# Kernel optimization log

Measured on AMD Instinct MI355X. Metric: run time of the kernel, lower is better.

Reference implementation:

```python
import jax, jax.numpy as jnp
import numpy as np

B, T, N = 2048, 500, 64
DT = 0.25  # integration step
V_TH = 30.0

# Izhikevich behaviour params: (a, b, c, d, v0); u0 = b * v0
LLBN_P = (0.02, 0.20, -65.0, 6.0, -70.0)   # LLBN_behaviour (tonic-spiking-like)
EBN_P  = (0.02, 0.25, -55.0, 0.05, -64.0)  # phasic bursting
IFN_P  = (0.02, 0.25, -65.0, 6.0, -64.0)   # phasic spiking
TN_P   = (0.02, 0.20, -50.0, 2.0, -70.0)   # tonic bursting
MN_P   = IFN_P                              # phasic spiking


def izh_step(v, u, I, p):
    """One Euler step of the Izhikevich neuron; returns (spike, v_new, u_new)."""
    a, b, c, d, _ = p
    v_ = v + DT * (0.04 * v * v + 5.0 * v + 140.0 - u + I)
    u_ = u + DT * a * (b * v - u)
    z = (v_ >= V_TH).astype(v.dtype)
    v_new = jnp.where(z > 0, c, v_)
    u_new = u_ + z * d
    return z, v_new, u_new


def init_state(p, batch):
    a, b, c, d, v0 = p
    return jnp.full((batch,), v0, jnp.float32), jnp.full((batch,), b * v0, jnp.float32)


def setup_inputs() -> dict:
    key = jax.random.key(0)
    k1, k2 = jax.random.split(key)
    input_mat = jax.random.uniform(k1, (B, T, N), dtype=jnp.float32)
    weights_matrix = jax.random.uniform(k2, (24,), dtype=jnp.float32)
    return {"input_mat": input_mat, "weights_matrix": weights_matrix}


def _run(input_mat, w):
    # summed retinal drive per timestep; [B, T] -> [T, B] for scan
    zp1 = (input_mat * w[0]).sum(-1).T
    zp2 = (input_mat * w[12]).sum(-1).T

    vL, uL = init_state(LLBN_P, B); zL = jnp.zeros((B,), jnp.float32)
    vE, uE = init_state(EBN_P, B)
    vI, uI = init_state(IFN_P, B)
    vT, uT = init_state(TN_P, B); zT = jnp.zeros((B,), jnp.float32)
    vM, uM = init_state(MN_P, B)
    # channel 2 uses the SAME cells (self.LLBN/EBN/... are reused in the
    # original forward, so weights w[2],w[3],w[9],w[10] apply) with its own state
    vL2, uL2 = vL, uL; zL2 = zL
    vE2, uE2 = vE, uE
    vI2, uI2 = vI, uI
    vT2, uT2 = vT, uT; zT2 = zT
    vM2, uM2 = vM, uM

    carry0 = (vL, uL, zL, vE, uE, vI, uI, vT, uT, zT, vM, uM,
              vL2, uL2, zL2, vE2, uE2, vI2, uI2, vT2, uT2, zT2, vM2, uM2)

    def step(carry, zin):
        (vL, uL, zL, vE, uE, vI, uI, vT, uT, zT, vM, uM,
         vL2, uL2, zL2, vE2, uE2, vI2, uI2, vT2, uT2, zT2, vM2, uM2) = carry
        zp, zp2 = zin
        # --- channel 1 ---  (temp feedback is always 0 in the original: local var)
        z2, vL, uL = izh_step(vL, uL, w[2] * (zp * w[1]) + w[3] * zL, LLBN_P)
        z3, vE, uE = izh_step(vE, uE, zp * w[4] + z2 * w[5], EBN_P)
        z4, vI, uI = izh_step(vI, uI, z3 * w[6], IFN_P)
        z5, vT, uT = izh_step(vT, uT, w[9] * (z3 * w[8]) + w[10] * zT, TN_P)
        z6, vM, uM = izh_step(vM, uM, z5 * w[11], MN_P)
        # --- channel 2 ---
        z22, vL2, uL2 = izh_step(vL2, uL2, w[2] * (zp2 * w[13]) + w[3] * zL2, LLBN_P)
        z32, vE2, uE2 = izh_step(vE2, uE2, zp2 * w[16] + z22 * w[17], EBN_P)
        z42, vI2, uI2 = izh_step(vI2, uI2, z32 * w[18], IFN_P)
        z52, vT2, uT2 = izh_step(vT2, uT2, w[9] * (z32 * w[20]) + w[10] * zT2, TN_P)
        z62, vM2, uM2 = izh_step(vM2, uM2, z52 * w[23], MN_P)
        new_carry = (vL, uL, z2, vE, uE, vI, uI, vT, uT, z5, vM, uM,
                     vL2, uL2, z22, vE2, uE2, vI2, uI2, vT2, uT2, z52, vM2, uM2)
        outs = (z6, vM, z62, vM2,
                jnp.stack([z2, z3, z4, z5], -1),   # o_spikes_o [B,4]
                jnp.stack([vL, vE, vI, vT], -1))   # v_o        [B,4]
        return new_carry, outs

    _, (o_spikes, v, o_spikes2, v2, o_spikes_o, v_o) = jax.lax.scan(step, carry0, (zp1, zp2))
    # scan stacks on leading T axis -> move to [B, T, ...]
    tr = lambda a: jnp.moveaxis(a, 0, 1)
    return tr(o_spikes), tr(v), tr(o_spikes2), tr(v2), tr(o_spikes_o), tr(v_o)


def reference(input_mat, weights_matrix):
    return _run(input_mat, weights_matrix)
```

## Files before the change

kernel.cpp:

```cpp
#include <hip/hip_runtime.h>

#define B_ 2048
#define T_ 500
#define BT (B_ * T_)

__device__ __forceinline__ float izh_m(float& v, float& u, float I,
                                       float b, float c, float d, bool valid) {
    float t  = 0.04f * v * v + 5.0f * v + 140.0f - u + I;
    float v_ = v + 0.25f * t;
    float u_ = u + 0.005f * (b * v - u);
    float z  = (v_ >= 30.0f) ? 1.0f : 0.0f;
    float vn = (v_ >= 30.0f) ? c : v_;
    float un = u_ + z * d;
    if (!valid) { z = 0.f; vn = v; un = u; }
    v = vn; u = un;
    return z;
}

__device__ __forceinline__ float dpp_shr1(float x) {
    return __int_as_float(__builtin_amdgcn_update_dpp(
        0, __float_as_int(x), 0x111, 0xf, 0xf, true));
}
__device__ __forceinline__ float dpp_shr2(float x) {
    return __int_as_float(__builtin_amdgcn_update_dpp(
        0, __float_as_int(x), 0x112, 0xf, 0xf, true));
}

#define BAR() do {                                                             \
    asm volatile("s_waitcnt lgkmcnt(0)" ::: "memory");                         \
    __builtin_amdgcn_s_barrier();                                              \
    __builtin_amdgcn_sched_barrier(0);                                         \
} while (0)

__global__ __launch_bounds__(128) void fused_scan4_kernel(
        const float* __restrict__ in, const float* __restrict__ w24,
        float* __restrict__ out) {
    __shared__ float S_lds[128];
    __shared__ float ring[32 * 56];

    const int tid   = threadIdx.x;
    const int wid   = tid >> 6;
    const int lane  = tid & 63;
    const int bbase = blockIdx.x << 2;

    const int c    = lane >> 4;
    const int slot = lane & 15;
    const int chl  = slot >> 3;
    const int role = slot & 7;

    const float a0   = chl ? w24[12] : w24[0];
    const float W1v  = chl ? w24[13] : w24[1];
    const float W4v  = chl ? w24[16] : w24[4];
    const float W5x  = chl ? w24[17] : w24[5];
    const float W6v  = chl ? w24[18] : w24[6];
    const float W8v  = chl ? w24[20] : w24[8];
    const float W11v = chl ? w24[23] : w24[11];
    const float W2 = w24[2], W3 = w24[3], W9 = w24[9], W10 = w24[10];

    float pb, pcc, pd, v, u, wA, wB, wC, wD;
    float fL = 0.f, fE = 0.f, fITM = 0.f;
    float sel1 = 0.f, sel2 = 0.f;
    int offs;
    if (role == 0) {
        pb=0.20f; pcc=-65.f; pd=6.f;   v=-70.f; u=-14.f;
        wA=W2;  wB=W1v;  wC=0.f; wD=W3;  offs=0; fL=1.f;
    } else if (role == 1) {
        pb=0.25f; pcc=-55.f; pd=0.05f; v=-64.f; u=-16.f;
        wA=1.f; wB=W4v;  wC=W5x; wD=0.f; offs=3; fE=1.f; sel1=1.f;
    } else if (role == 2) {
        pb=0.25f; pcc=-65.f; pd=6.f;   v=-64.f; u=-16.f;
        wA=1.f; wB=W6v;  wC=0.f; wD=0.f; offs=6; fITM=1.f; sel1=1.f;
    } else if (role == 3) {
        pb=0.20f; pcc=-50.f; pd=2.f;   v=-70.f; u=-14.f;
        wA=W9;  wB=W8v;  wC=0.f; wD=W10; offs=6; fITM=1.f; sel2=1.f;
    } else if (role == 4) {
        pb=0.25f; pcc=-65.f; pd=6.f;   v=-64.f; u=-16.f;
        wA=1.f; wB=W11v; wC=0.f; wD=0.f; offs=9; fITM=1.f; sel1=1.f;
    } else {
        pb=0.25f; pcc=-65.f; pd=6.f;   v=-64.f; u=-16.f;
        wA=0.f; wB=0.f;  wC=0.f; wD=0.f; offs=9;
    }
    const bool wr = (chl == 0 && role <= 4) || (chl == 1 && role == 4);
    const int  p  = (chl == 0) ? role : 5;
    const int ringoff = c * 14 + 2 * p;

    float z_last = 0.f, in_p1 = 0.f, in_p2 = 0.f;
    float zp1 = 0.f, zp2 = 0.f, zp3 = 0.f;

    const float* inb = in + (size_t)bbase * T_ * 64;
    float4 Ae[8], Ao[8], Be[8], Bo[8];

#define ISSUE(KK, BE, BO) {                                                    \
    const int t0i = 16 * (KK);                                                 \
    _Pragma("unroll")                                                          \
    for (int pp = 0; pp < 8; ++pp) {                                           \
        const int rt = pp * 8 + (lane >> 3);                                   \
        const int row = rt >> 4, tt = rt & 15;                                 \
        const int tcl = (t0i + tt <= 499) ? tt : 0;                            \
        const float* ap = inb + ((size_t)row * T_ + t0i + tcl) * 64            \
                              + (lane & 7) * 8;                                \
        BE[pp] = *(const float4*)ap;                                           \
        BO[pp] = *(const float4*)(ap + 4);                                     \
    }                                                                          \
}

#define REDUCE(KK, BE, BO) {                                                   \
    float* sw = S_lds + ((KK) & 1) * 64;                                       \
    const int t0r = 16 * (KK);                                                 \
    _Pragma("unroll")                                                          \
    for (int pp = 0; pp < 8; ++pp) {                                           \
        float4 e = BE[pp], o = BO[pp];                                         \
        float s = ((e.x + e.y) + (e.z + e.w)) + ((o.x + o.y) + (o.z + o.w));   \
        s += __shfl_xor(s, 1);                                                 \
        s += __shfl_xor(s, 2);                                                 \
        s += __shfl_xor(s, 4);                                                 \
        const int rt = pp * 8 + (lane >> 3);                                   \
        const int row = rt >> 4, tt = rt & 15;                                 \
        if ((lane & 7) == 0) sw[row * 16 + tt] = (t0r + tt <= 499) ? s : 0.f;  \
    }                                                                          \
}

#define SYS_ITER(SV, VEXPR, I_) {                                              \
    float in0 = in_p2;                                                         \
    in_p2 = in_p1;                                                             \
    {                                                                          \
        float s1_ = dpp_shr1(z_last);                                          \
        float s2_ = dpp_shr2(z_last);                                          \
        in_p1 = sel1 * s1_ + sel2 * s2_;                                       \
    }                                                                          \
    float zpc = (SV) * a0;                                                     \
    float X = (fL * zpc + fE * zp3) + fITM * in0;                              \
    float Isyn = wA * (X * wB) + wC * in0 + wD * z_last;                       \
    float znew = izh_m(v, u, Isyn, pb, pcc, pd, (VEXPR));                      \
    if (wr) *(float2*)(ringp + (I_) * 56) = make_float2(znew, v);              \
    zp3 = zp2; zp2 = zp1; zp1 = zpc;                                           \
    z_last = znew;                                                             \
}

#define GROUP16(VF)                                                            \
    SYS_ITER(g0.x, VF(0),  0)  SYS_ITER(g0.y, VF(1),  1)                       \
    SYS_ITER(g0.z, VF(2),  2)  SYS_ITER(g0.w, VF(3),  3)                       \
    SYS_ITER(g1.x, VF(4),  4)  SYS_ITER(g1.y, VF(5),  5)                       \
    SYS_ITER(g1.z, VF(6),  6)  SYS_ITER(g1.w, VF(7),  7)                       \
    SYS_ITER(g2.x, VF(8),  8)  SYS_ITER(g2.y, VF(9),  9)                       \
    SYS_ITER(g2.z, VF(10), 10) SYS_ITER(g2.w, VF(11), 11)                      \
    SYS_ITER(g3.x, VF(12), 12) SYS_ITER(g3.y, VF(13), 13)                      \
    SYS_ITER(g3.z, VF(14), 14) SYS_ITER(g3.w, VF(15), 15)

#define VF_PRO(i)  ((i) >= offs)
#define VF_ONE(i)  true
#define VF_EPI(i)  ((i) <= 3 + offs)

#define DUMP(K) {                                                              \
    const int td = lane & 15;                                                  \
    const int cc = lane >> 4;                                                  \
    const int t  = 16 * (K) - 9 + td;                                          \
    if (0 <= t && t <= 499) {                                                  \
        const float* rb = ring + cc * 14;                                      \
        float2 a2 = *(const float2*)&rb[((t)     & 31) * 56 + 0];              \
        float2 b2 = *(const float2*)&rb[((t + 3) & 31) * 56 + 2];              \
        float2 c1 = *(const float2*)&rb[((t + 6) & 31) * 56 + 4];              \
        float2 c2 = *(const float2*)&rb[((t + 6) & 31) * 56 + 6];              \
        float2 e1 = *(const float2*)&rb[((t + 9) & 31) * 56 + 8];              \
        float2 e2 = *(const float2*)&rb[((t + 9) & 31) * 56 + 10];             \
        const size_t g = (size_t)(bbase + cc) * T_ + t;                        \
        out[g]          = e1.x;                           \
        out[BT + g]     = e1.y;                           \
        out[2 * BT + g] = e2.x;                           \
        out[3 * BT + g] = e2.y;                           \
        ((float4*)out)[BT + g]     = make_float4(a2.x, b2.x, c1.x, c2.x);      \
        ((float4*)out)[2 * BT + g] = make_float4(a2.y, b2.y, c1.y, c2.y);      \
    }                                                                          \
}

#define SCANP(K, VFSEL) {                                                      \
    const float4* sp = (const float4*)(S_lds + ((K) & 1) * 64 + c * 16);       \
    float4 g0 = sp[0], g1 = sp[1], g2 = sp[2], g3 = sp[3];                     \
    float* ringp = ring + ((K) & 1) * 896 + ringoff;                           \
    GROUP16(VFSEL)                                                             \
    DUMP(K)                                                                    \
}

    if (wid == 1) {
        ISSUE(0, Ae, Ao)
        REDUCE(0, Ae, Ao)
        ISSUE(1, Be, Bo)
    }
    BAR();

    for (int k = 0; k < 32; k += 2) {
        if (wid == 0) {
            if (k == 0) { SCANP(k, VF_PRO) } else { SCANP(k, VF_ONE) }
        } else {
            if (k + 2 < 32) { ISSUE(k + 2, Ae, Ao) }
            if (k + 1 < 32) { REDUCE(k + 1, Be, Bo) }
        }
        BAR();
        if (wid == 0) {
            if (k + 1 == 31) { SCANP(k + 1, VF_EPI) } else { SCANP(k + 1, VF_ONE) }
        } else {
            if (k + 3 < 32) { ISSUE(k + 3, Be, Bo) }
            if (k + 2 < 32) { REDUCE(k + 2, Ae, Ao) }
        }
        BAR();
    }

#undef ISSUE
#undef REDUCE
#undef SYS_ITER
#undef GROUP16
#undef VF_PRO
#undef VF_ONE
#undef VF_EPI
#undef DUMP
#undef SCANP
}

extern "C" void kernel_launch(void* const* d_in, const int* in_sizes, int n_in,
                              void* d_out, int out_size, void* d_ws, size_t ws_size,
                              hipStream_t stream) {
    const float* in = (const float*)d_in[0];
    const float* w  = (const float*)d_in[1];
    float* out = (float*)d_out;

    fused_scan4_kernel<<<512, 128, 0, stream>>>(in, w, out);
}
```

Measured before the change: 73.22 us.

## Move output dump to loader wave and simplify neuron lane mapping

Output writes (DUMP) move from the scan wave to the loader wave, running one phase behind. The ring buffer grows to four slots so a slot is not overwritten before it is dumped. Lanes are remapped so every dependency is a shift-by-one DPP, which drops the second DPP and the select blend. The scan section gets raised wave priority. This takes global stores off the serial scan's critical path, at the cost of more LDS and more work for the loader wave.

```diff
diff --git a/kernel.cpp b/kernel.cpp
--- a/kernel.cpp
+++ b/kernel.cpp
@@ -21,10 +21,6 @@
     return __int_as_float(__builtin_amdgcn_update_dpp(
         0, __float_as_int(x), 0x111, 0xf, 0xf, true));
 }
-__device__ __forceinline__ float dpp_shr2(float x) {
-    return __int_as_float(__builtin_amdgcn_update_dpp(
-        0, __float_as_int(x), 0x112, 0xf, 0xf, true));
-}
 
 #define BAR() do {                                                             \
     asm volatile("s_waitcnt lgkmcnt(0)" ::: "memory");                         \
@@ -32,21 +28,21 @@
     __builtin_amdgcn_sched_barrier(0);                                         \
 } while (0)
 
-__global__ __launch_bounds__(128) void fused_scan4_kernel(
+__global__ __launch_bounds__(128) void fused_scan6_kernel(
         const float* __restrict__ in, const float* __restrict__ w24,
         float* __restrict__ out) {
     __shared__ float S_lds[128];
-    __shared__ float ring[32 * 56];
+    __shared__ float ring[64 * 56];
 
     const int tid   = threadIdx.x;
     const int wid   = tid >> 6;
     const int lane  = tid & 63;
     const int bbase = blockIdx.x << 2;
 
-    const int c    = lane >> 4;
-    const int slot = lane & 15;
-    const int chl  = slot >> 3;
-    const int role = slot & 7;
+    const int c     = lane >> 4;
+    const int slot  = lane & 15;
+    const int chl   = slot >> 3;
+    const int role8 = slot & 7;
 
     const float a0   = chl ? w24[12] : w24[0];
     const float W1v  = chl ? w24[13] : w24[1];
@@ -59,29 +55,33 @@
 
     float pb, pcc, pd, v, u, wA, wB, wC, wD;
     float fL = 0.f, fE = 0.f, fITM = 0.f;
-    float sel1 = 0.f, sel2 = 0.f;
     int offs;
-    if (role == 0) {
+    if (role8 == 0 || role8 == 4) {
         pb=0.20f; pcc=-65.f; pd=6.f;   v=-70.f; u=-14.f;
         wA=W2;  wB=W1v;  wC=0.f; wD=W3;  offs=0; fL=1.f;
-    } else if (role == 1) {
+    } else if (role8 == 1 || role8 == 5) {
         pb=0.25f; pcc=-55.f; pd=0.05f; v=-64.f; u=-16.f;
-        wA=1.f; wB=W4v;  wC=W5x; wD=0.f; offs=3; fE=1.f; sel1=1.f;
-    } else if (role == 2) {
+        wA=1.f; wB=W4v;  wC=W5x; wD=0.f; offs=3; fE=1.f;
+    } else if (role8 == 2) {
         pb=0.25f; pcc=-65.f; pd=6.f;   v=-64.f; u=-16.f;
-        wA=1.f; wB=W6v;  wC=0.f; wD=0.f; offs=6; fITM=1.f; sel1=1.f;
-    } else if (role == 3) {
+        wA=1.f; wB=W6v;  wC=0.f; wD=0.f; offs=6; fITM=1.f;
+    } else if (role8 == 6) {
         pb=0.20f; pcc=-50.f; pd=2.f;   v=-70.f; u=-14.f;
-        wA=W9;  wB=W8v;  wC=0.f; wD=W10; offs=6; fITM=1.f; sel2=1.f;
-    } else if (role == 4) {
+        wA=W9;  wB=W8v;  wC=0.f; wD=W10; offs=6; fITM=1.f;
+    } else if (role8 == 7) {
         pb=0.25f; pcc=-65.f; pd=6.f;   v=-64.f; u=-16.f;
-        wA=1.f; wB=W11v; wC=0.f; wD=0.f; offs=9; fITM=1.f; sel1=1.f;
+        wA=1.f; wB=W11v; wC=0.f; wD=0.f; offs=9; fITM=1.f;
     } else {
         pb=0.25f; pcc=-65.f; pd=6.f;   v=-64.f; u=-16.f;
         wA=0.f; wB=0.f;  wC=0.f; wD=0.f; offs=9;
     }
-    const bool wr = (chl == 0 && role <= 4) || (chl == 1 && role == 4);
-    const int  p  = (chl == 0) ? role : 5;
+    const bool wr = (chl == 0 && (role8 <= 2 || role8 == 6 || role8 == 7))
+                 || (chl == 1 && role8 == 7);
+    int p = 0;
+    if (role8 == 1) p = 1;
+    else if (role8 == 2) p = 2;
+    else if (role8 == 6) p = 3;
+    else if (role8 == 7) p = chl ? 5 : 4;
     const int ringoff = c * 14 + 2 * p;
 
     float z_last = 0.f, in_p1 = 0.f, in_p2 = 0.f;
@@ -123,11 +123,7 @@
 #define SYS_ITER(SV, VEXPR, I_) {                                              \
     float in0 = in_p2;                                                         \
     in_p2 = in_p1;                                                             \
-    {                                                                          \
-        float s1_ = dpp_shr1(z_last);                                          \
-        float s2_ = dpp_shr2(z_last);                                          \
-        in_p1 = sel1 * s1_ + sel2 * s2_;                                       \
-    }                                                                          \
+    in_p1 = dpp_shr1(z_last);                                                  \
     float zpc = (SV) * a0;                                                     \
     float X = (fL * zpc + fE * zp3) + fITM * in0;                              \
     float Isyn = wA * (X * wB) + wC * in0 + wD * z_last;                       \
@@ -157,12 +153,12 @@
     const int t  = 16 * (K) - 9 + td;                                          \
     if (0 <= t && t <= 499) {                                                  \
         const float* rb = ring + cc * 14;                                      \
-        float2 a2 = *(const float2*)&rb[((t)     & 31) * 56 + 0];              \
-        float2 b2 = *(const float2*)&rb[((t + 3) & 31) * 56 + 2];              \
-        float2 c1 = *(const float2*)&rb[((t + 6) & 31) * 56 + 4];              \
-        float2 c2 = *(const float2*)&rb[((t + 6) & 31) * 56 + 6];              \
-        float2 e1 = *(const float2*)&rb[((t + 9) & 31) * 56 + 8];              \
-        float2 e2 = *(const float2*)&rb[((t + 9) & 31) * 56 + 10];             \
+        float2 a2 = *(const float2*)&rb[((t)     & 63) * 56 + 0];              \
+        float2 b2 = *(const float2*)&rb[((t + 3) & 63) * 56 + 2];              \
+        float2 c1 = *(const float2*)&rb[((t + 6) & 63) * 56 + 4];              \
+        float2 c2 = *(const float2*)&rb[((t + 6) & 63) * 56 + 6];              \
+        float2 e1 = *(const float2*)&rb[((t + 9) & 63) * 56 + 8];              \
+        float2 e2 = *(const float2*)&rb[((t + 9) & 63) * 56 + 10];             \
         const size_t g = (size_t)(bbase + cc) * T_ + t;                        \
         out[g]          = e1.x;                           \
         out[BT + g]     = e1.y;                           \
@@ -176,9 +172,10 @@
 #define SCANP(K, VFSEL) {                                                      \
     const float4* sp = (const float4*)(S_lds + ((K) & 1) * 64 + c * 16);       \
     float4 g0 = sp[0], g1 = sp[1], g2 = sp[2], g3 = sp[3];                     \
-    float* ringp = ring + ((K) & 1) * 896 + ringoff;                           \
+    float* ringp = ring + ((K) & 3) * 896 + ringoff;                           \
+    __builtin_amdgcn_s_setprio(1);                                             \
     GROUP16(VFSEL)                                                             \
-    DUMP(K)                                                                    \
+    __builtin_amdgcn_s_setprio(0);                                             \
 }
 
     if (wid == 1) {
@@ -194,6 +191,7 @@
         } else {
             if (k + 2 < 32) { ISSUE(k + 2, Ae, Ao) }
             if (k + 1 < 32) { REDUCE(k + 1, Be, Bo) }
+            if (k >= 1) { DUMP(k - 1) }
         }
         BAR();
         if (wid == 0) {
@@ -201,9 +199,11 @@
         } else {
             if (k + 3 < 32) { ISSUE(k + 3, Be, Bo) }
             if (k + 2 < 32) { REDUCE(k + 2, Ae, Ao) }
+            DUMP(k)
         }
         BAR();
     }
+    if (wid == 1) { DUMP(31) }
 
 #undef ISSUE
 #undef REDUCE
@@ -223,5 +223,5 @@
     const float* w  = (const float*)d_in[1];
     float* out = (float*)d_out;
 
-    fused_scan4_kernel<<<512, 128, 0, stream>>>(in, w, out);
-}
+    fused_scan6_kernel<<<512, 128, 0, stream>>>(in, w, out);
+}
```

Result: no change. 72.54 us (-0.9%).
